# Kernel optimization log

Hardware: AMD Instinct MI355X
Metric: run time of the kernel (lower is better)

Reference implementation:

```python
import jax, jax.numpy as jnp
import numpy as np

# Haar (db1) analysis filters, already time-reversed as in create_wavelet_filter
# (for Haar the synthesis filters coincide with the analysis filters).
_S = 0.5
DEC = jnp.array([[[ _S,  _S], [ _S,  _S]],   # LL
                 [[ _S,  _S], [-_S, -_S]],   # LH (lo along w, hi along h)
                 [[ _S, -_S], [ _S, -_S]],   # HL
                 [[ _S, -_S], [-_S,  _S]]],  # HH
                dtype=jnp.float32)


def dwconv3(x, w, b=None):
    """Depthwise 3x3 'same' conv. x: [B,C,H,W], w: [C,3,3]."""
    c = x.shape[1]
    y = jax.lax.conv_general_dilated(
        x, w[:, None], (1, 1), 'SAME',
        feature_group_count=c,
        dimension_numbers=('NCHW', 'OIHW', 'NCHW'))
    if b is not None:
        y = y + b[None, :, None, None]
    return y


def haar_dwt(x):
    """Stride-2 grouped Haar DWT. [B,C,H,W] -> [B,C,4,H/2,W/2]."""
    b, c, h, w = x.shape
    xr = x.reshape(b, c, h // 2, 2, w // 2, 2)
    return jnp.einsum('bcipjq,kpq->bckij', xr, DEC)


def haar_idwt(y):
    """Inverse Haar (conv_transpose stride 2, kernel 2 => non-overlapping)."""
    b, c, _, h2, w2 = y.shape
    out = jnp.einsum('bckij,kpq->bcipjq', y, DEC)
    return out.reshape(b, c, h2 * 2, w2 * 2)


def ln_cf(x, w, b, eps=1e-6):
    """ConvNeXt channels-first LayerNorm (mean/var over channel dim)."""
    u = jnp.mean(x, axis=1, keepdims=True)
    s = jnp.mean((x - u) ** 2, axis=1, keepdims=True)
    xn = (x - u) / jnp.sqrt(s + eps)
    return w[None, :, None, None] * xn + b[None, :, None, None]


def wtconv_dw(x, base_w, base_b, base_s, wt_w, wt_s):
    """WTConv2d depthwise path, wt_levels=1, db1. x: [B,C,H,W] (H,W even)."""
    b, c, h, w = x.shape
    cx = haar_dwt(x)                                  # [B,C,4,H/2,W/2]
    tag = cx.reshape(b, c * 4, h // 2, w // 2)
    tag = dwconv3(tag, wt_w) * wt_s[None, :, None, None]
    x_tag = haar_idwt(tag.reshape(b, c, 4, h // 2, w // 2))
    base = dwconv3(x, base_w, base_b) * base_s[None, :, None, None]
    return base + x_tag


def resize_mat(n_in, n_out):
    """Bilinear align_corners=True interpolation matrix [n_out, n_in]."""
    coords = jnp.arange(n_out, dtype=jnp.float32) * ((n_in - 1) / (n_out - 1))
    i0 = jnp.clip(jnp.floor(coords).astype(jnp.int32), 0, n_in - 2)
    f = coords - i0.astype(jnp.float32)
    r = jnp.arange(n_out)
    return (jnp.zeros((n_out, n_in), jnp.float32)
            .at[r, i0].add(1.0 - f)
            .at[r, i0 + 1].add(f))


def setup_inputs() -> dict:
    key = jax.random.key(0)
    ks = jax.random.split(key, 16)
    B, C_XH, C_XL = 8, 16, 8
    HH, HL = 256, 512
    g = C_XL // 2 + 1        # per-branch channels = 5
    ct = 2 * C_XL + 4        # tail channels = 20
    n = jax.random.normal
    return {
        'xh': n(ks[0], (B, C_XH, HH, HH), jnp.float32),
        'xl': n(ks[1], (B, C_XL, HL, HL), jnp.float32),
        'mask': jax.random.uniform(ks[2], (B, 1, HL, HL), jnp.float32),
        'pre_w': n(ks[3], (C_XL, C_XH), jnp.float32) * 0.25,
        'pre_b': n(ks[4], (C_XL,), jnp.float32) * 0.1,
        'g_ln_w': jnp.ones((4, g), jnp.float32),
        'g_ln_b': jnp.zeros((4, g), jnp.float32),
        'g_base_w': n(ks[5], (4, g, 3, 3), jnp.float32) * 0.3,
        'g_base_b': n(ks[6], (4, g), jnp.float32) * 0.1,
        'g_base_s': jnp.ones((4, g), jnp.float32),
        'g_wt_w': n(ks[7], (4, 4 * g, 3, 3), jnp.float32) * 0.3,
        'g_wt_s': jnp.full((4, 4 * g), 0.1, jnp.float32),
        'g_pw_w': n(ks[8], (4, g, g), jnp.float32) * 0.3,
        'tail_ln_w': jnp.ones((ct,), jnp.float32),
        'tail_ln_b': jnp.zeros((ct,), jnp.float32),
        'tail_w': n(ks[9], (C_XL, ct), jnp.float32) * 0.2,
        'tail_b': n(ks[10], (C_XL,), jnp.float32) * 0.1,
        'res_w': n(ks[11], (C_XL, C_XL + 1), jnp.float32) * 0.3,
        'res_b': n(ks[12], (C_XL,), jnp.float32) * 0.1,
    }


def reference(xh, xl, mask, pre_w, pre_b, g_ln_w, g_ln_b, g_base_w, g_base_b,
              g_base_s, g_wt_w, g_wt_s, g_pw_w, tail_ln_w, tail_ln_b,
              tail_w, tail_b, res_w, res_b):
    # pre_project: 1x1 conv dim_xh -> dim_xl (with bias)
    xh_p = jnp.einsum('oc,bchw->bohw', pre_w, xh) + pre_b[None, :, None, None]
    # bilinear upsample to xl spatial size, align_corners=True (separable)
    Mh = resize_mat(xh.shape[2], xl.shape[2])
    Mw = resize_mat(xh.shape[3], xl.shape[3])
    xh_u = jnp.einsum('Hh,bchw,Ww->bcHW', Mh, xh_p, Mw)
    # four branches: chunk xh/xl, concat with mask, LN_cf -> WTConv dw -> 1x1
    gs = xl.shape[1] // 4   # channels per chunk (2)
    outs = []
    for i in range(4):
        gi = jnp.concatenate(
            [xh_u[:, i * gs:(i + 1) * gs], xl[:, i * gs:(i + 1) * gs], mask],
            axis=1)                                   # [B, gs*2+1, H, W]
        gi = ln_cf(gi, g_ln_w[i], g_ln_b[i])
        gi = wtconv_dw(gi, g_base_w[i], g_base_b[i], g_base_s[i],
                       g_wt_w[i], g_wt_s[i])
        gi = jnp.einsum('oc,bchw->bohw', g_pw_w[i], gi)  # pointwise, no bias
        outs.append(gi)
    x = jnp.concatenate(outs, axis=1)                 # [B, 2*dim_xl+4, H, W]
    # tail: LN_cf -> 1x1 conv -> exact GELU
    x = ln_cf(x, tail_ln_w, tail_ln_b)
    x = jnp.einsum('oc,bchw->bohw', tail_w, x) + tail_b[None, :, None, None]
    x = jax.nn.gelu(x, approximate=False)
    # residual: 1x1 conv on cat(xl, mask)
    res = jnp.einsum('oc,bchw->bohw', res_w,
                     jnp.concatenate([xl, mask], axis=1))
    res = res + res_b[None, :, None, None]
    return x + res
```

## Files before the change

kernel.cpp:

```cpp
#include <hip/hip_runtime.h>
#include <math.h>

#define BB   8
#define CXH  16
#define CXL  8
#define HH   256
#define HL   512

#define TS   32
#define HALO 2
#define GT   (TS + 2*HALO)
#define NPX  (GT * GT)

#define WS_PATCH_FLOATS (BB * 4 * HH * HH * 2)
#define WS_AB_OFF       WS_PATCH_FLOATS
#define WS_NEEDED_BYTES ((size_t)(WS_PATCH_FLOATS + 16) * sizeof(float))

__device__ __forceinline__ float gelu_fast(float x) {
    const float u = x * (1.595769122f + 0.071354816f * x * x);
    return x * __builtin_amdgcn_rcpf(1.0f + __expf(-u));
}

__device__ __forceinline__ void ln5(float* vv, const float* w, const float* bta) {
    const float u = (vv[0] + vv[1] + vv[2] + vv[3] + vv[4]) * 0.2f;
    float var = 0.f;
    #pragma unroll
    for (int c = 0; c < 5; ++c) { const float d = vv[c] - u; var += d * d; }
    var *= 0.2f;
    const float rstd = rsqrtf(var + 1e-6f);
    #pragma unroll
    for (int c = 0; c < 5; ++c) vv[c] = w[c] * ((vv[c] - u) * rstd) + bta[c];
}

__global__ __launch_bounds__(256)
void pre_project_kernel(const float* __restrict__ xh,
                        const float* __restrict__ pre_w,
                        const float* __restrict__ pre_b,
                        const float* __restrict__ tail_ln_w,
                        const float* __restrict__ tail_ln_b,
                        const float* __restrict__ tail_w,
                        const float* __restrict__ tail_b,
                        float* __restrict__ ws)
{
    const int gid = blockIdx.x * 256 + threadIdx.x;
    const int b   = gid >> 16;
    const int px  = gid & 0xFFFF;
    const float* xp = xh + (b * CXH) * (HH * HH) + px;
    float xv[16];
    #pragma unroll
    for (int c = 0; c < 16; ++c) xv[c] = xp[c * HH * HH];
    #pragma unroll
    for (int br = 0; br < 4; ++br) {
        float a0 = pre_b[2 * br], a1 = pre_b[2 * br + 1];
        #pragma unroll
        for (int c = 0; c < 16; ++c) {
            a0 += pre_w[(2 * br) * 16 + c] * xv[c];
            a1 += pre_w[(2 * br + 1) * 16 + c] * xv[c];
        }
        float2 r; r.x = a0; r.y = a1;
        *(float2*)&ws[((b * 4 + br) * (HH * HH) + px) * 2] = r;
    }
    if (gid < 8) {
        const int o = gid;
        float a = 0.f, bb = tail_b[o];
        for (int cg = 0; cg < 20; ++cg) {
            a  += tail_w[o * 20 + cg] * tail_ln_w[cg];
            bb += tail_w[o * 20 + cg] * tail_ln_b[cg];
        }
        ws[WS_AB_OFF + o]     = a;
        ws[WS_AB_OFF + 8 + o] = bb;
    }
}

__global__ __launch_bounds__(256, 3)
void uem_pair_kernel(const float* __restrict__ xl,
                     const float* __restrict__ mask,
                     const float* __restrict__ g_ln_w,
                     const float* __restrict__ g_ln_b,
                     const float* __restrict__ g_base_w,
                     const float* __restrict__ g_base_b,
                     const float* __restrict__ g_base_s,
                     const float* __restrict__ g_wt_w,
                     const float* __restrict__ g_wt_s,
                     const float* __restrict__ g_pw_w,
                     const float* __restrict__ tail_ln_w,
                     const float* __restrict__ tail_w,
                     const float* __restrict__ res_w,
                     const float* __restrict__ res_b,
                     const float* __restrict__ ws,
                     float* __restrict__ out)
{
    __shared__ __align__(16) float s_q[2][5][18][18][4];

    const int b   = blockIdx.z;
    const int ty0 = blockIdx.y * TS;
    const int tx0 = blockIdx.x * TS;
    const int tx  = threadIdx.x, ty = threadIdx.y;
    const int tid = ty * 16 + tx;

    const float SC = (float)(255.0 / 511.0);
    const int plane = HL * HL;
    const int mb  = b * plane;
    const int xlb = (b * CXL) * plane;

    float S1[4] = {0.f, 0.f, 0.f, 0.f};
    float S2[4] = {0.f, 0.f, 0.f, 0.f};
    float T[4][8];
    #pragma unroll
    for (int p = 0; p < 4; ++p)
        #pragma unroll
        for (int o = 0; o < 8; ++o) T[p][o] = 0.f;

    for (int pair = 0; pair < 2; ++pair) {
        const float* wsp0 = ws + ((size_t)(b * 4 + 2 * pair)     * (HH * HH)) * 2;
        const float* wsp1 = ws + ((size_t)(b * 4 + 2 * pair + 1) * (HH * HH)) * 2;
        int ly = tid / 36, lx = tid % 36;
        for (int idx = tid; idx < NPX; idx += 256) {
            const int gy = ty0 - HALO + ly, gx = tx0 - HALO + lx;
            float va[5] = {0.f, 0.f, 0.f, 0.f, 0.f};
            float vb[5] = {0.f, 0.f, 0.f, 0.f, 0.f};
            if (gy >= 0 && gy < HL && gx >= 0 && gx < HL) {
                const float cy = (float)gy * SC;
                const int iy0 = min((int)cy, HH - 2);
                const float fy = cy - (float)iy0;
                const float cx = (float)gx * SC;
                const int ix0 = min((int)cx, HH - 2);
                const float fx = cx - (float)ix0;
                const int co  = (iy0 * HH + ix0) * 2;
                const int pix = gy * HL + gx;
                const float mk = mask[mb + pix];
                {
                    const float2 q00 = *(const float2*)&wsp0[co];
                    const float2 q01 = *(const float2*)&wsp0[co + 2];
                    const float2 q10 = *(const float2*)&wsp0[co + 2 * HH];
                    const float2 q11 = *(const float2*)&wsp0[co + 2 * HH + 2];
                    {
                        const float top = q00.x + fx * (q01.x - q00.x);
                        const float bot = q10.x + fx * (q11.x - q10.x);
                        va[0] = top + fy * (bot - top);
                    }
                    {
                        const float top = q00.y + fx * (q01.y - q00.y);
                        const float bot = q10.y + fx * (q11.y - q10.y);
                        va[1] = top + fy * (bot - top);
                    }
                    va[2] = xl[xlb + (4 * pair + 0) * plane + pix];
                    va[3] = xl[xlb + (4 * pair + 1) * plane + pix];
                    va[4] = mk;
                    ln5(va, g_ln_w + (2 * pair) * 5, g_ln_b + (2 * pair) * 5);
                }
                {
                    const float2 q00 = *(const float2*)&wsp1[co];
                    const float2 q01 = *(const float2*)&wsp1[co + 2];
                    const float2 q10 = *(const float2*)&wsp1[co + 2 * HH];
                    const float2 q11 = *(const float2*)&wsp1[co + 2 * HH + 2];
                    {
                        const float top = q00.x + fx * (q01.x - q00.x);
                        const float bot = q10.x + fx * (q11.x - q10.x);
                        vb[0] = top + fy * (bot - top);
                    }
                    {
                        const float top = q00.y + fx * (q01.y - q00.y);
                        const float bot = q10.y + fx * (q11.y - q10.y);
                        vb[1] = top + fy * (bot - top);
                    }
                    vb[2] = xl[xlb + (4 * pair + 2) * plane + pix];
                    vb[3] = xl[xlb + (4 * pair + 3) * plane + pix];
                    vb[4] = mk;
                    ln5(vb, g_ln_w + (2 * pair + 1) * 5, g_ln_b + (2 * pair + 1) * 5);
                }
            }
            const int qy = ly >> 1, qx = lx >> 1, sub = (ly & 1) * 2 + (lx & 1);
            #pragma unroll
            for (int c = 0; c < 5; ++c) s_q[0][c][qy][qx][sub] = va[c];
            #pragma unroll
            for (int c = 0; c < 5; ++c) s_q[1][c][qy][qx][sub] = vb[c];
            lx += 4; ly += 7;
            if (lx >= 36) { lx -= 36; ly += 1; }
        }
        __syncthreads();

        for (int s = 0; s < 2; ++s) {
            const int br = 2 * pair + s;
            const float* wb = g_wt_w + br * 180;
            float gi[5][4];
            #pragma unroll
            for (int c = 0; c < 5; ++c) {
                float P[6][6];
                #pragma unroll
                for (int a = 0; a < 3; ++a)
                    #pragma unroll
                    for (int bq = 0; bq < 3; ++bq) {
                        const float4 q = *(const float4*)&s_q[s][c][ty + a][tx + bq][0];
                        P[2 * a][2 * bq]         = q.x;
                        P[2 * a][2 * bq + 1]     = q.y;
                        P[2 * a + 1][2 * bq]     = q.z;
                        P[2 * a + 1][2 * bq + 1] = q.w;
                    }
                float tc0 = 0.f, tc1 = 0.f, tc2 = 0.f, tc3 = 0.f;
                #pragma unroll
                for (int dy = 0; dy < 3; ++dy) {
                    #pragma unroll
                    for (int dx = 0; dx < 3; ++dx) {
                        const float a  = P[2 * dy][2 * dx];
                        const float b2 = P[2 * dy][2 * dx + 1];
                        const float c2 = P[2 * dy + 1][2 * dx];
                        const float d2 = P[2 * dy + 1][2 * dx + 1];
                        const float s0 = a + b2, s1 = c2 + d2;
                        const float d0 = a - b2, d1 = c2 - d2;
                        const int wo = dy * 3 + dx;
                        tc0 += wb[(c * 4 + 0) * 9 + wo] * (s0 + s1);
                        tc1 += wb[(c * 4 + 1) * 9 + wo] * (s0 - s1);
                        tc2 += wb[(c * 4 + 2) * 9 + wo] * (d0 + d1);
                        tc3 += wb[(c * 4 + 3) * 9 + wo] * (d0 - d1);
                    }
                }
                const float t0 = tc0 * (0.5f * g_wt_s[br * 20 + c * 4 + 0]);
                const float t1 = tc1 * (0.5f * g_wt_s[br * 20 + c * 4 + 1]);
                const float t2 = tc2 * (0.5f * g_wt_s[br * 20 + c * 4 + 2]);
                const float t3 = tc3 * (0.5f * g_wt_s[br * 20 + c * 4 + 3]);
                const float xt0 = 0.5f * (t0 + t1 + t2 + t3);
                const float xt1 = 0.5f * (t0 + t1 - t2 - t3);
                const float xt2 = 0.5f * (t0 - t1 + t2 - t3);
                const float xt3 = 0.5f * (t0 - t1 - t2 + t3);
                const float* bw = g_base_w + br * 45 + c * 9;
                const float bb2 = g_base_b[br * 5 + c], bs = g_base_s[br * 5 + c];
                #pragma unroll
                for (int p = 0; p < 4; ++p) {
                    const int py = p >> 1, px = p & 1;
                    float acc = 0.f;
                    #pragma unroll
                    for (int dy = 0; dy < 3; ++dy)
                        #pragma unroll
                        for (int dx = 0; dx < 3; ++dx)
                            acc += bw[dy * 3 + dx] * P[1 + py + dy][1 + px + dx];
                    const float xtv = (p == 0) ? xt0 : (p == 1) ? xt1 : (p == 2) ? xt2 : xt3;
                    gi[c][p] = (acc + bb2) * bs + xtv;
                }
            }

            #pragma unroll
            for (int o = 0; o < 5; ++o) {
                const int cg = br * 5 + o;
                float v[4];
                #pragma unroll
                for (int p = 0; p < 4; ++p) {
                    float vv = 0.f;
                    #pragma unroll
                    for (int c = 0; c < 5; ++c) vv += g_pw_w[br * 25 + o * 5 + c] * gi[c][p];
                    v[p] = vv;
                    S1[p] += vv;
                    S2[p] += vv * vv;
                }
                const float lw = tail_ln_w[cg];
                #pragma unroll
                for (int o8 = 0; o8 < 8; ++o8) {
                    const float w = tail_w[o8 * 20 + cg] * lw;
                    T[0][o8] += w * v[0];
                    T[1][o8] += w * v[1];
                    T[2][o8] += w * v[2];
                    T[3][o8] += w * v[3];
                }
            }
        }
        if (pair == 0) __syncthreads();
    }

    float A[8], Bc[8];
    #pragma unroll
    for (int o = 0; o < 8; ++o) {
        A[o]  = ws[WS_AB_OFF + o];
        Bc[o] = ws[WS_AB_OFF + 8 + o];
    }

    #pragma unroll
    for (int py = 0; py < 2; ++py) {
        const int p0 = py * 2, p1 = py * 2 + 1;
        const int gy  = ty0 + 2 * ty + py;
        const int gx0 = tx0 + 2 * tx;
        const float u0    = S1[p0] * 0.05f;
        const float u1    = S1[p1] * 0.05f;
        const float rstd0 = rsqrtf(S2[p0] * 0.05f - u0 * u0 + 1e-6f);
        const float rstd1 = rsqrtf(S2[p1] * 0.05f - u1 * u1 + 1e-6f);

        const int xbase = xlb + gy * HL + gx0;
        float2 xlv[8];
        #pragma unroll
        for (int c = 0; c < 8; ++c) xlv[c] = *(const float2*)&xl[xbase + c * plane];
        const float2 mk = *(const float2*)&mask[mb + gy * HL + gx0];

        #pragma unroll
        for (int o = 0; o < 8; ++o) {
            const float val0 = (T[p0][o] - u0 * A[o]) * rstd0 + Bc[o];
            const float val1 = (T[p1][o] - u1 * A[o]) * rstd1 + Bc[o];
            float r0 = res_b[o] + res_w[o * 9 + 8] * mk.x;
            float r1 = res_b[o] + res_w[o * 9 + 8] * mk.y;
            #pragma unroll
            for (int c = 0; c < 8; ++c) {
                r0 += res_w[o * 9 + c] * xlv[c].x;
                r1 += res_w[o * 9 + c] * xlv[c].y;
            }
            float2 ov;
            ov.x = gelu_fast(val0) + r0;
            ov.y = gelu_fast(val1) + r1;
            *(float2*)&out[xbase + o * plane] = ov;
        }
    }
}

extern "C" void kernel_launch(void* const* d_in, const int* in_sizes, int n_in,
                              void* d_out, int out_size, void* d_ws, size_t ws_size,
                              hipStream_t stream) {
    (void)in_sizes; (void)out_size;
    if (n_in < 19) return;
    const float* xh        = (const float*)d_in[0];
    const float* xl        = (const float*)d_in[1];
    const float* mask      = (const float*)d_in[2];
    const float* pre_w     = (const float*)d_in[3];
    const float* pre_b     = (const float*)d_in[4];
    const float* g_ln_w    = (const float*)d_in[5];
    const float* g_ln_b    = (const float*)d_in[6];
    const float* g_base_w  = (const float*)d_in[7];
    const float* g_base_b  = (const float*)d_in[8];
    const float* g_base_s  = (const float*)d_in[9];
    const float* g_wt_w    = (const float*)d_in[10];
    const float* g_wt_s    = (const float*)d_in[11];
    const float* g_pw_w    = (const float*)d_in[12];
    const float* tail_ln_w = (const float*)d_in[13];
    const float* tail_ln_b = (const float*)d_in[14];
    const float* tail_w    = (const float*)d_in[15];
    const float* tail_b    = (const float*)d_in[16];
    const float* res_w     = (const float*)d_in[17];
    const float* res_b     = (const float*)d_in[18];
    float* outp = (float*)d_out;
    float* ws   = (float*)d_ws;

    if (ws == nullptr || ws_size < WS_NEEDED_BYTES) return;

    pre_project_kernel<<<dim3(2048), dim3(256), 0, stream>>>(
        xh, pre_w, pre_b, tail_ln_w, tail_ln_b, tail_w, tail_b, ws);
    uem_pair_kernel<<<dim3(HL / TS, HL / TS, BB), dim3(16, 16, 1), 0, stream>>>(
        xl, mask, g_ln_w, g_ln_b, g_base_w, g_base_b, g_base_s,
        g_wt_w, g_wt_s, g_pw_w, tail_ln_w, tail_w, res_w, res_b, ws, outp);
}
```

Baseline: 296.6 us.

## Pair-pixel LDS staging, interior/edge specialization, and prefolded conv weights

The halo-tile fill now handles two horizontally adjacent pixels per task, using float2 loads for xl and mask and float2 LDS stores. Blocks that touch the image border are split from interior ones through a template, so interior tiles skip bounds checks and index clamps. The scale factors of the wavelet conv, base conv and tail conv are folded into packed weight tables in the workspace by the pre-projection kernel, which removes per-tap multiplies and scattered weight reads. This costs more workspace, more setup work in the first kernel, and a larger code footprint from two template instantiations.

```diff
diff --git a/kernel.cpp b/kernel.cpp
--- a/kernel.cpp
+++ b/kernel.cpp
@@ -10,11 +10,16 @@
 #define TS   32
 #define HALO 2
 #define GT   (TS + 2*HALO)
-#define NPX  (GT * GT)
+#define NPAIR (GT * GT / 2)
 
 #define WS_PATCH_FLOATS (BB * 4 * HH * HH * 2)
 #define WS_AB_OFF       WS_PATCH_FLOATS
-#define WS_NEEDED_BYTES ((size_t)(WS_PATCH_FLOATS + 16) * sizeof(float))
+#define WS_W2T_OFF      (WS_AB_OFF + 16)
+#define WS_WBS_OFF      (WS_W2T_OFF + 160)
+#define WS_BWS_OFF      (WS_WBS_OFF + 720)
+#define WS_BBS_OFF      (WS_BWS_OFF + 180)
+#define WS_TOTAL_FLOATS (WS_BBS_OFF + 20)
+#define WS_NEEDED_BYTES ((size_t)WS_TOTAL_FLOATS * sizeof(float))
 
 __device__ __forceinline__ float gelu_fast(float x) {
     const float u = x * (1.595769122f + 0.071354816f * x * x);
@@ -30,12 +35,35 @@
     const float rstd = rsqrtf(var + 1e-6f);
     #pragma unroll
     for (int c = 0; c < 5; ++c) vv[c] = w[c] * ((vv[c] - u) * rstd) + bta[c];
+}
+
+__device__ __forceinline__ void bil2(const float* __restrict__ wsp, int cbase,
+                                     float fx, float fy, float& o0, float& o1) {
+    const float2 q00 = *(const float2*)&wsp[cbase];
+    const float2 q01 = *(const float2*)&wsp[cbase + 2];
+    const float2 q10 = *(const float2*)&wsp[cbase + 2 * HH];
+    const float2 q11 = *(const float2*)&wsp[cbase + 2 * HH + 2];
+    {
+        const float top = q00.x + fx * (q01.x - q00.x);
+        const float bot = q10.x + fx * (q11.x - q10.x);
+        o0 = top + fy * (bot - top);
+    }
+    {
+        const float top = q00.y + fx * (q01.y - q00.y);
+        const float bot = q10.y + fx * (q11.y - q10.y);
+        o1 = top + fy * (bot - top);
+    }
 }
 
 __global__ __launch_bounds__(256)
 void pre_project_kernel(const float* __restrict__ xh,
                         const float* __restrict__ pre_w,
                         const float* __restrict__ pre_b,
+                        const float* __restrict__ g_base_w,
+                        const float* __restrict__ g_base_b,
+                        const float* __restrict__ g_base_s,
+                        const float* __restrict__ g_wt_w,
+                        const float* __restrict__ g_wt_s,
                         const float* __restrict__ tail_ln_w,
                         const float* __restrict__ tail_ln_b,
                         const float* __restrict__ tail_w,
@@ -69,6 +97,102 @@
         }
         ws[WS_AB_OFF + o]     = a;
         ws[WS_AB_OFF + 8 + o] = bb;
+    } else if (gid < 8 + 160) {
+        const int i = gid - 8;
+        const int cg = i / 8, o8 = i % 8;
+        ws[WS_W2T_OFF + i] = tail_w[o8 * 20 + cg] * tail_ln_w[cg];
+    } else if (gid < 8 + 160 + 720) {
+        const int i = gid - 168;
+        const int wo = i % 9;
+        const int rest = i / 9;
+        const int k = rest % 4;
+        const int bc = rest / 4;
+        const int br = bc / 5, c = bc % 5;
+        ws[WS_WBS_OFF + i] =
+            g_wt_w[br * 180 + (c * 4 + k) * 9 + wo] * (0.5f * g_wt_s[br * 20 + c * 4 + k]);
+    } else if (gid < 8 + 160 + 720 + 180) {
+        const int i = gid - 888;
+        const int wo = i % 9;
+        const int bc = i / 9;
+        const int br = bc / 5, c = bc % 5;
+        ws[WS_BWS_OFF + i] = g_base_w[br * 45 + c * 9 + wo] * g_base_s[bc];
+    } else if (gid < 8 + 160 + 720 + 180 + 20) {
+        const int i = gid - 1068;
+        ws[WS_BBS_OFF + i] = g_base_b[i] * g_base_s[i];
+    }
+}
+
+template <bool EDGE>
+__device__ __forceinline__ void build_pair_lds(
+    float (&s_q)[2][5][18][18][4],
+    int tid, int ty0, int tx0, int mb, int xlb, int pair,
+    const float* __restrict__ xl, const float* __restrict__ mask,
+    const float* __restrict__ g_ln_w, const float* __restrict__ g_ln_b,
+    const float* __restrict__ wsp0, const float* __restrict__ wsp1)
+{
+    const float SC = (float)(255.0 / 511.0);
+    const int plane = HL * HL;
+    const float* gwA = g_ln_w + (2 * pair) * 5;
+    const float* gbA = g_ln_b + (2 * pair) * 5;
+    const float* gwB = g_ln_w + (2 * pair + 1) * 5;
+    const float* gbB = g_ln_b + (2 * pair + 1) * 5;
+
+    int r = tid / 18, m = tid % 18;
+    for (int task = tid; task < NPAIR; task += 256) {
+        const int gy  = ty0 - HALO + r;
+        const int gx0 = tx0 - HALO + 2 * m;
+        float a0[5] = {0,0,0,0,0}, a1[5] = {0,0,0,0,0};
+        float b0[5] = {0,0,0,0,0}, b1[5] = {0,0,0,0,0};
+        bool ok = true;
+        if (EDGE) ok = (gy >= 0) && (gy < HL) && (gx0 >= 0) && (gx0 < HL);
+        if (ok) {
+            const float cy = (float)gy * SC;
+            int iy0 = (int)cy;
+            if (EDGE) iy0 = min(iy0, HH - 2);
+            const float fy = cy - (float)iy0;
+            const float cx0 = (float)gx0 * SC;
+            int ix00 = (int)cx0;
+            if (EDGE) ix00 = min(ix00, HH - 2);
+            const float fx0 = cx0 - (float)ix00;
+            const float cx1 = (float)(gx0 + 1) * SC;
+            int ix01 = (int)cx1;
+            if (EDGE) ix01 = min(ix01, HH - 2);
+            const float fx1 = cx1 - (float)ix01;
+            const int c0 = (iy0 * HH + ix00) * 2;
+            const int c1 = (iy0 * HH + ix01) * 2;
+            const int pix = gy * HL + gx0;
+            const float2 mk = *(const float2*)&mask[mb + pix];
+
+            bil2(wsp0, c0, fx0, fy, a0[0], a0[1]);
+            bil2(wsp0, c1, fx1, fy, a1[0], a1[1]);
+            bil2(wsp1, c0, fx0, fy, b0[0], b0[1]);
+            bil2(wsp1, c1, fx1, fy, b1[0], b1[1]);
+
+            const float2 x0 = *(const float2*)&xl[xlb + (4 * pair + 0) * plane + pix];
+            const float2 x1 = *(const float2*)&xl[xlb + (4 * pair + 1) * plane + pix];
+            const float2 x2 = *(const float2*)&xl[xlb + (4 * pair + 2) * plane + pix];
+            const float2 x3 = *(const float2*)&xl[xlb + (4 * pair + 3) * plane + pix];
+            a0[2] = x0.x; a1[2] = x0.y; a0[3] = x1.x; a1[3] = x1.y;
+            a0[4] = mk.x; a1[4] = mk.y;
+            b0[2] = x2.x; b1[2] = x2.y; b0[3] = x3.x; b1[3] = x3.y;
+            b0[4] = mk.x; b1[4] = mk.y;
+
+            ln5(a0, gwA, gbA); ln5(a1, gwA, gbA);
+            ln5(b0, gwB, gbB); ln5(b1, gwB, gbB);
+        }
+        const int qy = r >> 1, sub0 = (r & 1) * 2;
+        #pragma unroll
+        for (int c = 0; c < 5; ++c) {
+            float2 t; t.x = a0[c]; t.y = a1[c];
+            *(float2*)&s_q[0][c][qy][m][sub0] = t;
+        }
+        #pragma unroll
+        for (int c = 0; c < 5; ++c) {
+            float2 t; t.x = b0[c]; t.y = b1[c];
+            *(float2*)&s_q[1][c][qy][m][sub0] = t;
+        }
+        m += 4; r += 14;
+        if (m >= 18) { m -= 18; r += 1; }
     }
 }
 
@@ -77,14 +201,7 @@
                      const float* __restrict__ mask,
                      const float* __restrict__ g_ln_w,
                      const float* __restrict__ g_ln_b,
-                     const float* __restrict__ g_base_w,
-                     const float* __restrict__ g_base_b,
-                     const float* __restrict__ g_base_s,
-                     const float* __restrict__ g_wt_w,
-                     const float* __restrict__ g_wt_s,
                      const float* __restrict__ g_pw_w,
-                     const float* __restrict__ tail_ln_w,
-                     const float* __restrict__ tail_w,
                      const float* __restrict__ res_w,
                      const float* __restrict__ res_b,
                      const float* __restrict__ ws,
@@ -97,8 +214,9 @@
     const int tx0 = blockIdx.x * TS;
     const int tx  = threadIdx.x, ty = threadIdx.y;
     const int tid = ty * 16 + tx;
-
-    const float SC = (float)(255.0 / 511.0);
+    const bool edge = (blockIdx.x == 0) || (blockIdx.x == gridDim.x - 1) ||
+                      (blockIdx.y == 0) || (blockIdx.y == gridDim.y - 1);
+
     const int plane = HL * HL;
     const int mb  = b * plane;
     const int xlb = (b * CXL) * plane;
@@ -114,75 +232,19 @@
     for (int pair = 0; pair < 2; ++pair) {
         const float* wsp0 = ws + ((size_t)(b * 4 + 2 * pair)     * (HH * HH)) * 2;
         const float* wsp1 = ws + ((size_t)(b * 4 + 2 * pair + 1) * (HH * HH)) * 2;
-        int ly = tid / 36, lx = tid % 36;
-        for (int idx = tid; idx < NPX; idx += 256) {
-            const int gy = ty0 - HALO + ly, gx = tx0 - HALO + lx;
-            float va[5] = {0.f, 0.f, 0.f, 0.f, 0.f};
-            float vb[5] = {0.f, 0.f, 0.f, 0.f, 0.f};
-            if (gy >= 0 && gy < HL && gx >= 0 && gx < HL) {
-                const float cy = (float)gy * SC;
-                const int iy0 = min((int)cy, HH - 2);
-                const float fy = cy - (float)iy0;
-                const float cx = (float)gx * SC;
-                const int ix0 = min((int)cx, HH - 2);
-                const float fx = cx - (float)ix0;
-                const int co  = (iy0 * HH + ix0) * 2;
-                const int pix = gy * HL + gx;
-                const float mk = mask[mb + pix];
-                {
-                    const float2 q00 = *(const float2*)&wsp0[co];
-                    const float2 q01 = *(const float2*)&wsp0[co + 2];
-                    const float2 q10 = *(const float2*)&wsp0[co + 2 * HH];
-                    const float2 q11 = *(const float2*)&wsp0[co + 2 * HH + 2];
-                    {
-                        const float top = q00.x + fx * (q01.x - q00.x);
-                        const float bot = q10.x + fx * (q11.x - q10.x);
-                        va[0] = top + fy * (bot - top);
-                    }
-                    {
-                        const float top = q00.y + fx * (q01.y - q00.y);
-                        const float bot = q10.y + fx * (q11.y - q10.y);
-                        va[1] = top + fy * (bot - top);
-                    }
-                    va[2] = xl[xlb + (4 * pair + 0) * plane + pix];
-                    va[3] = xl[xlb + (4 * pair + 1) * plane + pix];
-                    va[4] = mk;
-                    ln5(va, g_ln_w + (2 * pair) * 5, g_ln_b + (2 * pair) * 5);
-                }
-                {
-                    const float2 q00 = *(const float2*)&wsp1[co];
-                    const float2 q01 = *(const float2*)&wsp1[co + 2];
-                    const float2 q10 = *(const float2*)&wsp1[co + 2 * HH];
-                    const float2 q11 = *(const float2*)&wsp1[co + 2 * HH + 2];
-                    {
-                        const float top = q00.x + fx * (q01.x - q00.x);
-                        const float bot = q10.x + fx * (q11.x - q10.x);
-                        vb[0] = top + fy * (bot - top);
-                    }
-                    {
-                        const float top = q00.y + fx * (q01.y - q00.y);
-                        const float bot = q10.y + fx * (q11.y - q10.y);
-                        vb[1] = top + fy * (bot - top);
-                    }
-                    vb[2] = xl[xlb + (4 * pair + 2) * plane + pix];
-                    vb[3] = xl[xlb + (4 * pair + 3) * plane + pix];
-                    vb[4] = mk;
-                    ln5(vb, g_ln_w + (2 * pair + 1) * 5, g_ln_b + (2 * pair + 1) * 5);
-                }
-            }
-            const int qy = ly >> 1, qx = lx >> 1, sub = (ly & 1) * 2 + (lx & 1);
-            #pragma unroll
-            for (int c = 0; c < 5; ++c) s_q[0][c][qy][qx][sub] = va[c];
-            #pragma unroll
-            for (int c = 0; c < 5; ++c) s_q[1][c][qy][qx][sub] = vb[c];
-            lx += 4; ly += 7;
-            if (lx >= 36) { lx -= 36; ly += 1; }
-        }
+        if (edge)
+            build_pair_lds<true >(s_q, tid, ty0, tx0, mb, xlb, pair,
+                                  xl, mask, g_ln_w, g_ln_b, wsp0, wsp1);
+        else
+            build_pair_lds<false>(s_q, tid, ty0, tx0, mb, xlb, pair,
+                                  xl, mask, g_ln_w, g_ln_b, wsp0, wsp1);
         __syncthreads();
 
         for (int s = 0; s < 2; ++s) {
             const int br = 2 * pair + s;
-            const float* wb = g_wt_w + br * 180;
+            const float* wbs = ws + WS_WBS_OFF + (size_t)(br * 5) * 36;
+            const float* bws = ws + WS_BWS_OFF + (size_t)(br * 5) * 9;
+            const float* bbs = ws + WS_BBS_OFF + br * 5;
             float gi[5][4];
             #pragma unroll
             for (int c = 0; c < 5; ++c) {
@@ -197,7 +259,8 @@
                         P[2 * a + 1][2 * bq]     = q.z;
                         P[2 * a + 1][2 * bq + 1] = q.w;
                     }
-                float tc0 = 0.f, tc1 = 0.f, tc2 = 0.f, tc3 = 0.f;
+                const float* wc = wbs + c * 36;
+                float t0 = 0.f, t1 = 0.f, t2 = 0.f, t3 = 0.f;
                 #pragma unroll
                 for (int dy = 0; dy < 3; ++dy) {
                     #pragma unroll
@@ -209,33 +272,29 @@
                         const float s0 = a + b2, s1 = c2 + d2;
                         const float d0 = a - b2, d1 = c2 - d2;
                         const int wo = dy * 3 + dx;
-                        tc0 += wb[(c * 4 + 0) * 9 + wo] * (s0 + s1);
-                        tc1 += wb[(c * 4 + 1) * 9 + wo] * (s0 - s1);
-                        tc2 += wb[(c * 4 + 2) * 9 + wo] * (d0 + d1);
-                        tc3 += wb[(c * 4 + 3) * 9 + wo] * (d0 - d1);
+                        t0 += wc[wo]      * (s0 + s1);
+                        t1 += wc[9 + wo]  * (s0 - s1);
+                        t2 += wc[18 + wo] * (d0 + d1);
+                        t3 += wc[27 + wo] * (d0 - d1);
                     }
                 }
-                const float t0 = tc0 * (0.5f * g_wt_s[br * 20 + c * 4 + 0]);
-                const float t1 = tc1 * (0.5f * g_wt_s[br * 20 + c * 4 + 1]);
-                const float t2 = tc2 * (0.5f * g_wt_s[br * 20 + c * 4 + 2]);
-                const float t3 = tc3 * (0.5f * g_wt_s[br * 20 + c * 4 + 3]);
                 const float xt0 = 0.5f * (t0 + t1 + t2 + t3);
                 const float xt1 = 0.5f * (t0 + t1 - t2 - t3);
                 const float xt2 = 0.5f * (t0 - t1 + t2 - t3);
                 const float xt3 = 0.5f * (t0 - t1 - t2 + t3);
-                const float* bw = g_base_w + br * 45 + c * 9;
-                const float bb2 = g_base_b[br * 5 + c], bs = g_base_s[br * 5 + c];
+                const float* bwc = bws + c * 9;
+                const float bc = bbs[c];
                 #pragma unroll
                 for (int p = 0; p < 4; ++p) {
                     const int py = p >> 1, px = p & 1;
-                    float acc = 0.f;
+                    float acc = bc;
                     #pragma unroll
                     for (int dy = 0; dy < 3; ++dy)
                         #pragma unroll
                         for (int dx = 0; dx < 3; ++dx)
-                            acc += bw[dy * 3 + dx] * P[1 + py + dy][1 + px + dx];
+                            acc += bwc[dy * 3 + dx] * P[1 + py + dy][1 + px + dx];
                     const float xtv = (p == 0) ? xt0 : (p == 1) ? xt1 : (p == 2) ? xt2 : xt3;
-                    gi[c][p] = (acc + bb2) * bs + xtv;
+                    gi[c][p] = acc + xtv;
                 }
             }
 
@@ -252,10 +311,10 @@
                     S1[p] += vv;
                     S2[p] += vv * vv;
                 }
-                const float lw = tail_ln_w[cg];
+                const float* w2 = ws + WS_W2T_OFF + cg * 8;
                 #pragma unroll
                 for (int o8 = 0; o8 < 8; ++o8) {
-                    const float w = tail_w[o8 * 20 + cg] * lw;
+                    const float w = w2[o8];
                     T[0][o8] += w * v[0];
                     T[1][o8] += w * v[1];
                     T[2][o8] += w * v[2];
@@ -267,10 +326,15 @@
     }
 
     float A[8], Bc[8];
-    #pragma unroll
-    for (int o = 0; o < 8; ++o) {
-        A[o]  = ws[WS_AB_OFF + o];
-        Bc[o] = ws[WS_AB_OFF + 8 + o];
+    {
+        const float4 a0 = *(const float4*)&ws[WS_AB_OFF];
+        const float4 a1 = *(const float4*)&ws[WS_AB_OFF + 4];
+        const float4 b0 = *(const float4*)&ws[WS_AB_OFF + 8];
+        const float4 b1 = *(const float4*)&ws[WS_AB_OFF + 12];
+        A[0]=a0.x; A[1]=a0.y; A[2]=a0.z; A[3]=a0.w;
+        A[4]=a1.x; A[5]=a1.y; A[6]=a1.z; A[7]=a1.w;
+        Bc[0]=b0.x; Bc[1]=b0.y; Bc[2]=b0.z; Bc[3]=b0.w;
+        Bc[4]=b1.x; Bc[5]=b1.y; Bc[6]=b1.z; Bc[7]=b1.w;
     }
 
     #pragma unroll
@@ -338,8 +402,8 @@
     if (ws == nullptr || ws_size < WS_NEEDED_BYTES) return;
 
     pre_project_kernel<<<dim3(2048), dim3(256), 0, stream>>>(
-        xh, pre_w, pre_b, tail_ln_w, tail_ln_b, tail_w, tail_b, ws);
+        xh, pre_w, pre_b, g_base_w, g_base_b, g_base_s, g_wt_w, g_wt_s,
+        tail_ln_w, tail_ln_b, tail_w, tail_b, ws);
     uem_pair_kernel<<<dim3(HL / TS, HL / TS, BB), dim3(16, 16, 1), 0, stream>>>(
-        xl, mask, g_ln_w, g_ln_b, g_base_w, g_base_b, g_base_s,
-        g_wt_w, g_wt_s, g_pw_w, tail_ln_w, tail_w, res_w, res_b, ws, outp);
-}
+        xl, mask, g_ln_w, g_ln_b, g_pw_w, res_w, res_b, ws, outp);
+}
```

Result: faster. 287.3 us (-3.1%).
